# Optimization experiments

Hardware: AMD Instinct MI355X
Metric: run time of the kernel (lower is better)

The kernel has to match this reference:

```python
import jax, jax.numpy as jnp
import numpy as np

H, C, G, DIM = 8, 16, 32, 3
G3 = G ** 3
EPS = 1e-5
# corner offsets of the trilinear cell: [8, 3]
_OFFS = jnp.array([[i, j, k] for i in (0, 1) for j in (0, 1) for k in (0, 1)], dtype=jnp.int32)


def _bn(x, gamma, beta, mean, var):
    # eval-mode BatchNorm1d: x [B, Ch, N], params [Ch]
    inv = jax.lax.rsqrt(var + EPS)
    return (x - mean[:, None]) * (inv * gamma)[:, None] + beta[:, None]


def _lattice_coords(lattice):
    # lattice: [B, H, 3, N] in (-1, 1) -> flat indices [B,H,8,N], trilinear weights [B,H,8,N]
    pos = (lattice + 1.0) * (0.5 * (G - 1))
    base = jnp.clip(jnp.floor(pos), 0.0, G - 2)
    frac = pos - base                                   # [B,H,3,N]
    base = base.astype(jnp.int32)
    corner = base[:, :, None, :, :] + _OFFS[None, None, :, :, None]   # [B,H,8,3,N]
    flat_idx = (corner[:, :, :, 0] * G + corner[:, :, :, 1]) * G + corner[:, :, :, 2]
    w = jnp.where(_OFFS[None, None, :, :, None] == 1,
                  frac[:, :, None, :, :], 1.0 - frac[:, :, None, :, :])  # [B,H,8,3,N]
    weights = jnp.prod(w, axis=3)                       # [B,H,8,N]
    return flat_idx, weights


def _splat(values, flat_idx, weights):
    # values [B,H,C,N] -> lattice [B,H,C,G3] via weighted scatter-add over 8 corners
    N = values.shape[-1]
    def one(v, idx, w):  # v [C,N], idx/w [8,N]
        contrib = (v[:, None, :] * w[None, :, :]).reshape(C, 8 * N)
        return jnp.zeros((C, G3), v.dtype).at[:, idx.reshape(-1)].add(contrib)
    return jax.vmap(jax.vmap(one))(values, flat_idx, weights)


def _slice(grid, flat_idx, weights):
    # grid [B,H,C,G3] -> per-point features [B,H,C,N] via weighted gather over 8 corners
    N = flat_idx.shape[-1]
    def one(g, idx, w):
        gathered = g[:, idx.reshape(-1)].reshape(C, 8, N)
        return jnp.sum(gathered * w[None, :, :], axis=1)
    return jax.vmap(jax.vmap(one))(grid, flat_idx, weights)


def setup_inputs() -> dict:
    key = jax.random.key(0)
    ks = jax.random.split(key, 20)
    B, D, N = 4, 64, 16384
    inp = {
        "x": jax.random.normal(ks[0], (B, D, N), jnp.float32),
        "orig_points": jax.random.normal(ks[1], (B, 3, N), jnp.float32),
        "w_kv": jax.random.normal(ks[2], (H * (C + 3), D), jnp.float32) * 0.1,
        "kbn_gamma": jax.random.normal(ks[3], (H * 3,), jnp.float32) * 0.1,
        "kbn_beta": jax.random.normal(ks[4], (H * 3,), jnp.float32) * 0.1,
        "kbn_mean": jax.random.normal(ks[5], (H * 3,), jnp.float32) * 0.1,
        "kbn_var": jax.random.uniform(ks[6], (H * 3,), jnp.float32, 0.5, 1.5),
        "vbn_gamma": jax.random.normal(ks[7], (H * C,), jnp.float32),
        "vbn_beta": jax.random.normal(ks[8], (H * C,), jnp.float32) * 0.1,
        "vbn_mean": jax.random.normal(ks[9], (H * C,), jnp.float32) * 0.1,
        "vbn_var": jax.random.uniform(ks[10], (H * C,), jnp.float32, 0.5, 1.5),
        "Wt": jnp.eye(3, dtype=jnp.float32)[None] + jax.random.normal(ks[11], (H, 3, 3), jnp.float32) * 0.05,
        "bt": jax.random.normal(ks[12], (H, 3), jnp.float32) * 0.1,
        "conv_w": jax.random.normal(ks[13], (H * C, C, 3, 3, 3), jnp.float32) * 0.05,
        "conv_b": jax.random.normal(ks[14], (H * C,), jnp.float32) * 0.05,
        "abn_gamma": jax.random.normal(ks[15], (H * C,), jnp.float32),
        "abn_beta": jax.random.normal(ks[16], (H * C,), jnp.float32) * 0.1,
        "abn_mean": jax.random.normal(ks[17], (H * C,), jnp.float32) * 0.1,
        "abn_var": jax.random.uniform(ks[18], (H * C,), jnp.float32, 0.5, 1.5),
    }
    return inp


def reference(x, orig_points, w_kv, kbn_gamma, kbn_beta, kbn_mean, kbn_var,
              vbn_gamma, vbn_beta, vbn_mean, vbn_var, Wt, bt, conv_w, conv_b,
              abn_gamma, abn_beta, abn_mean, abn_var):
    B, D, N = x.shape
    kv = jnp.einsum('od,bdn->bon', w_kv, x)                       # [B, H*(C+3), N]
    keys_off = _bn(kv[:, :H * 3], kbn_gamma, kbn_beta, kbn_mean, kbn_var)
    values = _bn(kv[:, H * 3:], vbn_gamma, vbn_beta, vbn_mean, vbn_var)
    keys_off = keys_off.reshape(B, H, 3, N)
    pts = orig_points[:, None, :, :] + keys_off                   # [B,H,3,N]
    tkeys = jnp.einsum('hij,bhjn->bhin', Wt, pts) + bt[None, :, :, None]
    lattice = jnp.tanh(tkeys)                                     # [B,H,3,N]
    flat_idx, weights = _lattice_coords(lattice)
    vals = values.reshape(B, H, C, N)
    grid = _splat(vals, flat_idx, weights).reshape(B, H * C, G, G, G)
    conv = jax.lax.conv_general_dilated(
        grid, conv_w, (1, 1, 1), 'SAME',
        dimension_numbers=('NCDHW', 'OIDHW', 'NCDHW'),
        feature_group_count=H) + conv_b[None, :, None, None, None]
    sliced = _slice(conv.reshape(B, H, C, G3), flat_idx, weights)  # [B,H,C,N]
    out = _bn(sliced.reshape(B, H * C, N), abn_gamma, abn_beta, abn_mean, abn_var)
    return jax.nn.relu(out)
```

## Files before the change

### kernel.cpp

```cpp
#include <hip/hip_runtime.h>
#include <hip/hip_bf16.h>

#define NB  4
#define NH  8
#define NC  16
#define ND  64
#define NN  16384
#define NG  32
#define NG3 32768
#define NKV 152
#define KEPS 1e-5f
#define TN  256

typedef __attribute__((ext_vector_type(8))) short bf16x8;
typedef __attribute__((ext_vector_type(4))) float f32x4;

__device__ __forceinline__ unsigned pack_bf2(float lo, float hi) {
    __hip_bfloat16 a = __float2bfloat16(lo);
    __hip_bfloat16 b = __float2bfloat16(hi);
    return (unsigned)(*(unsigned short*)&a) | ((unsigned)(*(unsigned short*)&b) << 16);
}
__device__ __forceinline__ float bf_lo(unsigned u) { return __uint_as_float(u << 16); }
__device__ __forceinline__ float bf_hi(unsigned u) { return __uint_as_float(u & 0xffff0000u); }

__global__ __launch_bounds__(256)
void k_zero(uint4* __restrict__ p)
{
    p[(long)blockIdx.x * 256 + threadIdx.x] = make_uint4(0, 0, 0, 0);
}

__global__ __launch_bounds__(256)
void k_front4(const float* __restrict__ x,
              const float* __restrict__ orig,
              const float* __restrict__ wkv,
              const float* __restrict__ kg, const float* __restrict__ kb,
              const float* __restrict__ km, const float* __restrict__ kvv,
              const float* __restrict__ vg, const float* __restrict__ vb,
              const float* __restrict__ vm, const float* __restrict__ vv,
              const float* __restrict__ Wt,
              const float* __restrict__ bt,
              unsigned short* __restrict__ valb,
              float4* __restrict__ pre,
              int* __restrict__ hist)
{
    __shared__ unsigned short xb[TN * 72];
    __shared__ float wk[6 * ND];
    __shared__ float ksc[6], ksh[6], vsc[32], vsh[32], wts[18], bts[6];
    const int tid = threadIdx.x;
    const int hg   = blockIdx.x & 3;
    const int tile = (blockIdx.x >> 2) & 63;
    const int b    = blockIdx.x >> 8;
    const int n0 = tile * TN;
    const int n  = n0 + tid;

    for (int i = tid; i < 6 * ND; i += 256) wk[i] = wkv[hg * 384 + i];
    if (tid < 6) {
        int ch = hg * 6 + tid;
        float s = rsqrtf(kvv[ch] + KEPS) * kg[ch];
        ksc[tid] = s;
        ksh[tid] = kb[ch] - km[ch] * s;
    }
    if (tid < 32) {
        int ch = hg * 32 + tid;
        float s = rsqrtf(vv[ch] + KEPS) * vg[ch];
        vsc[tid] = s;
        vsh[tid] = vb[ch] - vm[ch] * s;
    }
    if (tid < 18) wts[tid] = Wt[hg * 18 + tid];
    if (tid < 6)  bts[tid] = bt[hg * 6 + tid];

    float xr[ND];
    #pragma unroll
    for (int d = 0; d < ND; ++d)
        xr[d] = x[((long)b * ND + d) * NN + n];
    #pragma unroll
    for (int j = 0; j < 8; ++j) {
        uint4 q;
        q.x = pack_bf2(xr[8*j+0], xr[8*j+1]);
        q.y = pack_bf2(xr[8*j+2], xr[8*j+3]);
        q.z = pack_bf2(xr[8*j+4], xr[8*j+5]);
        q.w = pack_bf2(xr[8*j+6], xr[8*j+7]);
        *(uint4*)(xb + tid * 72 + j * 8) = q;
    }
    __syncthreads();

    float ko[6];
    #pragma unroll 1
    for (int o = 0; o < 6; o += 3) {
        float s0 = 0.f, s1 = 0.f, s2 = 0.f;
        #pragma unroll
        for (int dq = 0; dq < 16; ++dq) {
            const float4 w0 = *(const float4*)&wk[(o + 0) * ND + dq * 4];
            const float4 w1 = *(const float4*)&wk[(o + 1) * ND + dq * 4];
            const float4 w2 = *(const float4*)&wk[(o + 2) * ND + dq * 4];
            float a0 = xr[4*dq], a1 = xr[4*dq+1], a2 = xr[4*dq+2], a3 = xr[4*dq+3];
            s0 = fmaf(w0.x, a0, fmaf(w0.y, a1, fmaf(w0.z, a2, fmaf(w0.w, a3, s0))));
            s1 = fmaf(w1.x, a0, fmaf(w1.y, a1, fmaf(w1.z, a2, fmaf(w1.w, a3, s1))));
            s2 = fmaf(w2.x, a0, fmaf(w2.y, a1, fmaf(w2.z, a2, fmaf(w2.w, a3, s2))));
        }
        ko[o + 0] = fmaf(s0, ksc[o + 0], ksh[o + 0]);
        ko[o + 1] = fmaf(s1, ksc[o + 1], ksh[o + 1]);
        ko[o + 2] = fmaf(s2, ksc[o + 2], ksh[o + 2]);
    }

    {
        const int lane = tid & 63;
        const int wv = tid >> 6;
        const int l15 = lane & 15, l4 = lane >> 4;
        const int hl = wv & 1;
        const int h = hg * 2 + hl;
        const int ocg = h * 16 + l15;
        const int nbr = (wv >> 1) * 8;
        const float bsc = vsc[hl * 16 + l15];
        const float bsh = vsh[hl * 16 + l15];

        bf16x8 bfr[2];
        #pragma unroll
        for (int ks = 0; ks < 2; ++ks) {
            const float* wp = wkv + (24 + ocg) * ND + ks * 32 + l4 * 8;
            float4 a = *(const float4*)wp;
            float4 c = *(const float4*)(wp + 4);
            uint4 q;
            q.x = pack_bf2(a.x, a.y); q.y = pack_bf2(a.z, a.w);
            q.z = pack_bf2(c.x, c.y); q.w = pack_bf2(c.z, c.w);
            bfr[ks] = *(bf16x8*)&q;
        }

        #pragma unroll 1
        for (int nbi = 0; nbi < 8; ++nbi) {
            int nb = nbr + nbi;
            bf16x8 a0 = *(const bf16x8*)(xb + (nb * 16 + l15) * 72 + l4 * 8);
            bf16x8 a1 = *(const bf16x8*)(xb + (nb * 16 + l15) * 72 + 32 + l4 * 8);
            f32x4 acc = (f32x4){0.f, 0.f, 0.f, 0.f};
            acc = __builtin_amdgcn_mfma_f32_16x16x32_bf16(a0, bfr[0], acc, 0, 0, 0);
            acc = __builtin_amdgcn_mfma_f32_16x16x32_bf16(a1, bfr[1], acc, 0, 0, 0);
            unsigned short* vp = valb + (((long)(b * NH + h) * NN + n0 + nb * 16 + l4 * 4) * NC) + l15;
            #pragma unroll
            for (int r = 0; r < 4; ++r) {
                __hip_bfloat16 hb = __float2bfloat16(fmaf(acc[r], bsc, bsh));
                vp[r * NC] = *(unsigned short*)&hb;
            }
        }
    }

    const float o0 = orig[((long)b * 3 + 0) * NN + n];
    const float o1 = orig[((long)b * 3 + 1) * NN + n];
    const float o2 = orig[((long)b * 3 + 2) * NN + n];

    #pragma unroll 1
    for (int lh = 0; lh < 2; ++lh) {
        float p0 = o0 + ko[lh * 3 + 0];
        float p1 = o1 + ko[lh * 3 + 1];
        float p2 = o2 + ko[lh * 3 + 2];
        float t0 = fmaf(wts[lh * 9 + 0], p0, fmaf(wts[lh * 9 + 1], p1, fmaf(wts[lh * 9 + 2], p2, bts[lh * 3 + 0])));
        float t1 = fmaf(wts[lh * 9 + 3], p0, fmaf(wts[lh * 9 + 4], p1, fmaf(wts[lh * 9 + 5], p2, bts[lh * 3 + 1])));
        float t2 = fmaf(wts[lh * 9 + 6], p0, fmaf(wts[lh * 9 + 7], p1, fmaf(wts[lh * 9 + 8], p2, bts[lh * 3 + 2])));
        float l0 = tanhf(t0), l1 = tanhf(t1), l2 = tanhf(t2);
        float pos0 = (l0 + 1.f) * 15.5f;
        float pos1 = (l1 + 1.f) * 15.5f;
        float pos2 = (l2 + 1.f) * 15.5f;
        float b0 = fminf(fmaxf(floorf(pos0), 0.f), 30.f);
        float b1 = fminf(fmaxf(floorf(pos1), 0.f), 30.f);
        float b2 = fminf(fmaxf(floorf(pos2), 0.f), 30.f);
        int ix = (int)b0, iy = (int)b1, iz = (int)b2;
        float fx = pos0 - b0, fy = pos1 - b1, fz = pos2 - b2;
        int ibase = (ix * NG + iy) * NG + iz;
        float4 pr;
        pr.x = __int_as_float(ibase);
        pr.y = fx; pr.z = fy; pr.w = fz;
        int bh = b * NH + hg * 2 + lh;
        pre[(long)bh * NN + n] = pr;
        atomicAdd(&hist[bh * NG3 + ibase], 1);
    }
}

__global__ __launch_bounds__(1024)
void k_scan_cells(const int* __restrict__ hist, int* __restrict__ offs,
                  int* __restrict__ offs_live)
{
    __shared__ int tsum[1024];
    const int bh = blockIdx.x, tid = threadIdx.x;
    const int* hb = hist + (long)bh * NG3;

    int s = 0;
    #pragma unroll 4
    for (int j = 0; j < 32; ++j) s += hb[tid * 32 + j];
    tsum[tid] = s;
    __syncthreads();
    for (int d = 1; d < 1024; d <<= 1) {
        int t = (tid >= d) ? tsum[tid - d] : 0;
        __syncthreads();
        tsum[tid] += t;
        __syncthreads();
    }
    int run = bh * NN + tsum[tid] - s;
    int* ob = offs + (long)bh * NG3;
    int* lb = offs_live + (long)bh * NG3;
    #pragma unroll 4
    for (int j = 0; j < 32; ++j) {
        int c = tid * 32 + j;
        ob[c] = run;
        lb[c] = run;
        run += hb[c];
    }
}

__global__ __launch_bounds__(256)
void k_scatter2(const float4* __restrict__ pre, const unsigned short* __restrict__ valb,
                int* __restrict__ offs_live, uint4* __restrict__ rec)
{
    const int bh   = 8 * ((blockIdx.x >> 3) & 3) + (blockIdx.x & 7);
    const int tile = blockIdx.x >> 5;
    long t = (long)bh * NN + tile * 256 + threadIdx.x;
    float4 r = pre[t];
    int ibase = __float_as_int(r.x);
    int slot = atomicAdd(&offs_live[(long)bh * NG3 + ibase], 1);
    const uint4* vp = (const uint4*)(valb + t * NC);
    uint4 v0 = vp[0], v1 = vp[1];
    uint4* out = rec + (long)slot * 3;
    out[0] = make_uint4(__float_as_uint(r.y), __float_as_uint(r.z), __float_as_uint(r.w), 0u);
    out[1] = v0;
    out[2] = v1;
}

__global__ __launch_bounds__(1024)
void k_splat6(const uint4* __restrict__ rec, const int* __restrict__ hist,
              const int* __restrict__ offs, unsigned short* __restrict__ gridb)
{
    __shared__ uint4 sr[1024 * 3];
    const int tid = threadIdx.x;
    const int bh = blockIdx.x & 31;
    const int rx = blockIdx.x >> 5;
    const int y = tid >> 5, z = tid & 31;
    const int zlo = (z > 0) ? z - 1 : 0;

    const int* hb = hist + (long)bh * NG3;
    const int* ob = offs + (long)bh * NG3;

    float acc[16];
    #pragma unroll
    for (int c = 0; c < 16; ++c) acc[c] = 0.f;

    #pragma unroll
    for (int dx = 0; dx < 2; ++dx) {
        int cx = rx - dx;
        if (cx < 0) continue;
        int st[2], sp[2], en[2];
        #pragma unroll
        for (int dy = 0; dy < 2; ++dy) {
            int cy = y - dy;
            bool valid = cy >= 0;
            int base = (cx << 10) | (cy << 5);
            int c1 = base | zlo;
            int c2 = base | z;
            st[dy] = valid ? ob[c1] : 0;
            sp[dy] = valid ? ob[c2] : 0;
            en[dy] = valid ? sp[dy] + hb[c2] : 0;
        }
        int pc0 = cx << 10;
        int ps = ob[pc0];
        int pe = ob[pc0 + 1023] + hb[pc0 + 1023];
        for (int cs = ps; cs < pe; cs += 1024) {
            int ce = min(cs + 1024, pe);
            __syncthreads();
            if (tid < ce - cs) {
                const uint4* R = rec + (long)(cs + tid) * 3;
                sr[tid * 3 + 0] = R[0];
                sr[tid * 3 + 1] = R[1];
                sr[tid * 3 + 2] = R[2];
            }
            __syncthreads();
            #pragma unroll
            for (int dy = 0; dy < 2; ++dy) {
                int ls = max(st[dy], cs);
                int le = min(en[dy], ce);
                int split = sp[dy];
                for (int r = ls; r < le; ++r) {
                    int k = (r - cs) * 3;
                    uint4 q0 = sr[k], q1 = sr[k + 1], q2 = sr[k + 2];
                    float fx = __uint_as_float(q0.x);
                    float fy = __uint_as_float(q0.y);
                    float fz = __uint_as_float(q0.z);
                    float wx = dx ? fx : 1.f - fx;
                    float wy = dy ? fy : 1.f - fy;
                    float wz = (r < split) ? fz : 1.f - fz;
                    float w = wx * wy * wz;
                    acc[0]  = fmaf(w, bf_lo(q1.x), acc[0]);
                    acc[1]  = fmaf(w, bf_hi(q1.x), acc[1]);
                    acc[2]  = fmaf(w, bf_lo(q1.y), acc[2]);
                    acc[3]  = fmaf(w, bf_hi(q1.y), acc[3]);
                    acc[4]  = fmaf(w, bf_lo(q1.z), acc[4]);
                    acc[5]  = fmaf(w, bf_hi(q1.z), acc[5]);
                    acc[6]  = fmaf(w, bf_lo(q1.w), acc[6]);
                    acc[7]  = fmaf(w, bf_hi(q1.w), acc[7]);
                    acc[8]  = fmaf(w, bf_lo(q2.x), acc[8]);
                    acc[9]  = fmaf(w, bf_hi(q2.x), acc[9]);
                    acc[10] = fmaf(w, bf_lo(q2.y), acc[10]);
                    acc[11] = fmaf(w, bf_hi(q2.y), acc[11]);
                    acc[12] = fmaf(w, bf_lo(q2.z), acc[12]);
                    acc[13] = fmaf(w, bf_hi(q2.z), acc[13]);
                    acc[14] = fmaf(w, bf_lo(q2.w), acc[14]);
                    acc[15] = fmaf(w, bf_hi(q2.w), acc[15]);
                }
            }
        }
    }

    uint4 q0, q1;
    q0.x = pack_bf2(acc[0],  acc[1]);  q0.y = pack_bf2(acc[2],  acc[3]);
    q0.z = pack_bf2(acc[4],  acc[5]);  q0.w = pack_bf2(acc[6],  acc[7]);
    q1.x = pack_bf2(acc[8],  acc[9]);  q1.y = pack_bf2(acc[10], acc[11]);
    q1.z = pack_bf2(acc[12], acc[13]); q1.w = pack_bf2(acc[14], acc[15]);
    uint4* gb = (uint4*)(gridb + ((long)bh * NG3 + (rx << 10) + tid) * NC);
    gb[0] = q0;
    gb[1] = q1;
}

__global__ __launch_bounds__(256)
void k_wprep(const float* __restrict__ cw, unsigned short* __restrict__ wpre)
{
    const int h = blockIdx.x;
    for (int e = threadIdx.x; e < 7168; e += 256) {
        int icl = e & 7, oc = (e >> 3) & 15, ihl = (e >> 7) & 1, tap = e >> 8;
        int ic = ihl * 8 + icl;
        float wv = (tap < 27) ? cw[(h * 16 + oc) * 432 + ic * 27 + tap] : 0.f;
        __hip_bfloat16 hbw = __float2bfloat16(wv);
        wpre[h * 7168 + e] = *(unsigned short*)&hbw;
    }
}

__global__ __launch_bounds__(512)
void k_conv5(const unsigned short* __restrict__ gridb,
             const unsigned short* __restrict__ wpre,
             const float* __restrict__ cb,
             unsigned short* __restrict__ convo)
{
    __shared__ unsigned short sg[2 * 6 * 10 * 34 * 8];
    __shared__ unsigned short sw[28 * 2 * 16 * 8];
    const int tid = threadIdx.x;
    const int bid = blockIdx.x;
    const int yt = bid & 3, xt = (bid >> 2) & 7, bh = bid >> 5;
    const int h = bh & 7;
    const int x0 = xt * 4, y0 = yt * 8;

    {
        const uint4* wsrc = (const uint4*)(wpre + (long)h * 7168);
        uint4* wdst = (uint4*)sw;
        for (int e = tid; e < 896; e += 512) wdst[e] = wsrc[e];
    }
    const unsigned short* gb = gridb + (long)bh * NG3 * 16;
    for (int e = tid; e < 2 * 6 * 10 * 34; e += 512) {
        int ihl = e & 1, c = e >> 1;
        int zz = c % 34, yu = c / 34;
        int yy = yu % 10, xx = yu / 10;
        int gx = x0 + xx - 1, gy = y0 + yy - 1, gz = zz - 1;
        uint4 v = make_uint4(0, 0, 0, 0);
        if ((unsigned)gx < NG && (unsigned)gy < NG && (unsigned)gz < NG)
            v = *(const uint4*)(gb + (((gx * NG + gy) * NG + gz) * 16 + ihl * 8));
        *(uint4*)(sg + ((((ihl * 6 + xx) * 10 + yy) * 34) + zz) * 8) = v;
    }
    __syncthreads();

    const int lane = tid & 63;
    const int w  = tid >> 6;
    const int wv = w & 3;
    const int zh = w >> 2;
    const int m  = lane & 15;
    const int l4 = lane >> 4;
    const int ihl = l4 & 1;
    const int tp = l4 >> 1;

    const int aLaneByte = ((((ihl * 6 + wv) * 10) * 34) + zh * 16 + m) * 16;
    const int bLaneByte = l4 * 256 + m * 16;
    const char* sgb = (const char*)sg;
    const char* swb = (const char*)sw;

    f32x4 acc[8];
    #pragma unroll
    for (int j = 0; j < 8; ++j) acc[j] = (f32x4){0.f, 0.f, 0.f, 0.f};

    #pragma unroll
    for (int p = 0; p < 14; ++p) {
        const int t0 = 2 * p, t1 = 2 * p + 1;
        const int ta0 = (t0 > 26) ? 26 : t0, ta1 = (t1 > 26) ? 26 : t1;
        const int off0 = ((ta0 / 9) * 340 + ((ta0 % 9) / 3) * 34 + (ta0 % 3)) * 16;
        const int off1 = ((ta1 / 9) * 340 + ((ta1 % 9) / 3) * 34 + (ta1 % 3)) * 16;
        const int aoff = aLaneByte + (tp ? off1 : off0);
        bf16x8 bfr = *(const bf16x8*)(swb + p * 1024 + bLaneByte);
        #pragma unroll
        for (int j = 0; j < 8; ++j) {
            bf16x8 afr = *(const bf16x8*)(sgb + aoff + j * 544);
            acc[j] = __builtin_amdgcn_mfma_f32_16x16x32_bf16(afr, bfr, acc[j], 0, 0, 0);
        }
    }

    const float bias = cb[h * 16 + m];
    unsigned short* cvb = convo + (long)bh * NG3 * NC;
    const int gx = x0 + wv;
    const int z0 = zh * 16;
    #pragma unroll
    for (int j = 0; j < 8; ++j) {
        int gy = y0 + j;
        long cellbase = (long)(gx * NG + gy) * NG + z0 + l4 * 4;
        #pragma unroll
        for (int r = 0; r < 4; ++r) {
            __hip_bfloat16 hb = __float2bfloat16(acc[j][r] + bias);
            cvb[(cellbase + r) * NC + m] = *(unsigned short*)&hb;
        }
    }
}

__global__ __launch_bounds__(256)
void k_slice(const unsigned short* __restrict__ convo, const float4* __restrict__ pre,
             const float* __restrict__ ag, const float* __restrict__ ab,
             const float* __restrict__ am, const float* __restrict__ av,
             float* __restrict__ out)
{
    __shared__ float asc[128], ash[128];
    const int tid = threadIdx.x;
    if (tid < 128) {
        float s = rsqrtf(av[tid] + KEPS) * ag[tid];
        asc[tid] = s;
        ash[tid] = ab[tid] - am[tid] * s;
    }
    __syncthreads();

    const int bh   = 8 * ((blockIdx.x >> 3) & 3) + (blockIdx.x & 7);
    const int tile = blockIdx.x >> 5;
    const int n = tile * 256 + tid;
    long t = (long)bh * NN + n;
    int b = bh >> 3, h = bh & 7;
    const unsigned short* g = convo + (long)bh * NG3 * NC;

    float4 r = pre[t];
    int ibase = __float_as_int(r.x);
    float fx = r.y, fy = r.z, fz = r.w;
    float gx = 1.f - fx, gy = 1.f - fy, gz = 1.f - fz;
    const float ws8[8] = {gx*gy*gz, gx*gy*fz, gx*fy*gz, gx*fy*fz,
                          fx*gy*gz, fx*gy*fz, fx*fy*gz, fx*fy*fz};
    const int offs8[8] = {0, 1, NG, NG + 1, NG*NG, NG*NG + 1, NG*NG + NG, NG*NG + NG + 1};

    float acc[NC];
    #pragma unroll
    for (int c = 0; c < NC; ++c) acc[c] = 0.f;
    #pragma unroll
    for (int ci = 0; ci < 8; ++ci) {
        float w = ws8[ci];
        const uint4* gc = (const uint4*)(g + (long)(ibase + offs8[ci]) * NC);
        uint4 u0 = gc[0], u1 = gc[1];
        acc[0]  = fmaf(w, bf_lo(u0.x), acc[0]);
        acc[1]  = fmaf(w, bf_hi(u0.x), acc[1]);
        acc[2]  = fmaf(w, bf_lo(u0.y), acc[2]);
        acc[3]  = fmaf(w, bf_hi(u0.y), acc[3]);
        acc[4]  = fmaf(w, bf_lo(u0.z), acc[4]);
        acc[5]  = fmaf(w, bf_hi(u0.z), acc[5]);
        acc[6]  = fmaf(w, bf_lo(u0.w), acc[6]);
        acc[7]  = fmaf(w, bf_hi(u0.w), acc[7]);
        acc[8]  = fmaf(w, bf_lo(u1.x), acc[8]);
        acc[9]  = fmaf(w, bf_hi(u1.x), acc[9]);
        acc[10] = fmaf(w, bf_lo(u1.y), acc[10]);
        acc[11] = fmaf(w, bf_hi(u1.y), acc[11]);
        acc[12] = fmaf(w, bf_lo(u1.z), acc[12]);
        acc[13] = fmaf(w, bf_hi(u1.z), acc[13]);
        acc[14] = fmaf(w, bf_lo(u1.w), acc[14]);
        acc[15] = fmaf(w, bf_hi(u1.w), acc[15]);
    }
    float* ob = out + ((long)b * 128 + h * 16) * NN + n;
    #pragma unroll
    for (int c = 0; c < NC; ++c) {
        float rr = fmaf(acc[c], asc[h * 16 + c], ash[h * 16 + c]);
        ob[(long)c * NN] = fmaxf(rr, 0.f);
    }
}

extern "C" void kernel_launch(void* const* d_in, const int* in_sizes, int n_in,
                              void* d_out, int out_size, void* d_ws, size_t ws_size,
                              hipStream_t stream)
{
    (void)in_sizes; (void)n_in; (void)out_size; (void)ws_size;
    const float* x    = (const float*)d_in[0];
    const float* orig = (const float*)d_in[1];
    const float* wkv  = (const float*)d_in[2];
    const float* kg   = (const float*)d_in[3];
    const float* kb   = (const float*)d_in[4];
    const float* km   = (const float*)d_in[5];
    const float* kvv  = (const float*)d_in[6];
    const float* vg   = (const float*)d_in[7];
    const float* vb   = (const float*)d_in[8];
    const float* vm   = (const float*)d_in[9];
    const float* vv   = (const float*)d_in[10];
    const float* Wt   = (const float*)d_in[11];
    const float* bt   = (const float*)d_in[12];
    const float* cw   = (const float*)d_in[13];
    const float* cb   = (const float*)d_in[14];
    const float* ag   = (const float*)d_in[15];
    const float* ab   = (const float*)d_in[16];
    const float* am   = (const float*)d_in[17];
    const float* av   = (const float*)d_in[18];

    char* ws = (char*)d_ws;
    float4*         pre       = (float4*)        (ws);
    int*            hist      = (int*)           (ws + 8388608);
    int*            offs      = (int*)           (ws + 12582912);
    int*            offs_live = (int*)           (ws + 16777216);
    unsigned short* valb      = (unsigned short*)(ws + 20971520);
    uint4*          rec       = (uint4*)         (ws + 37748736);
    unsigned short* gridb     = (unsigned short*)(ws + 62914560);
    unsigned short* wpre      = (unsigned short*)(ws + 96468992);
    unsigned short* convo     = (unsigned short*)(ws + 20971520);

    k_zero<<<dim3(1024), dim3(256), 0, stream>>>((uint4*)hist);

    k_wprep<<<dim3(NH), dim3(256), 0, stream>>>(cw, wpre);

    k_front4<<<dim3(NB * 256), dim3(256), 0, stream>>>(
        x, orig, wkv, kg, kb, km, kvv, vg, vb, vm, vv, Wt, bt, valb, pre, hist);

    k_scan_cells<<<dim3(NB * NH), dim3(1024), 0, stream>>>(hist, offs, offs_live);

    k_scatter2<<<dim3((NB * NH * NN) / 256), dim3(256), 0, stream>>>(
        pre, valb, offs_live, rec);

    k_splat6<<<dim3(NB * NH * NG), dim3(1024), 0, stream>>>(rec, hist, offs, gridb);

    k_conv5<<<dim3(NB * NH * 32), dim3(512), 0, stream>>>(gridb, wpre, cb, convo);

    k_slice<<<dim3((NB * NH * NN) / 256), dim3(256), 0, stream>>>(
        convo, pre, ag, ab, am, av, (float*)d_out);
}
```

Measured before the change: 195.6 us.

## Splat two x-planes per block to reuse loaded cell records

```diff
diff --git a/kernel.cpp b/kernel.cpp
--- a/kernel.cpp
+++ b/kernel.cpp
@@ -224,40 +224,42 @@
 }
 
 __global__ __launch_bounds__(1024)
-void k_splat6(const uint4* __restrict__ rec, const int* __restrict__ hist,
+void k_splat7(const uint4* __restrict__ rec, const int* __restrict__ hist,
               const int* __restrict__ offs, unsigned short* __restrict__ gridb)
 {
     __shared__ uint4 sr[1024 * 3];
     const int tid = threadIdx.x;
     const int bh = blockIdx.x & 31;
-    const int rx = blockIdx.x >> 5;
+    const int kp = blockIdx.x >> 5;
     const int y = tid >> 5, z = tid & 31;
     const int zlo = (z > 0) ? z - 1 : 0;
 
     const int* hb = hist + (long)bh * NG3;
     const int* ob = offs + (long)bh * NG3;
 
-    float acc[16];
-    #pragma unroll
-    for (int c = 0; c < 16; ++c) acc[c] = 0.f;
-
-    #pragma unroll
-    for (int dx = 0; dx < 2; ++dx) {
-        int cx = rx - dx;
-        if (cx < 0) continue;
+    float acc0[16], acc1[16];
+    #pragma unroll
+    for (int c = 0; c < 16; ++c) { acc0[c] = 0.f; acc1[c] = 0.f; }
+
+    #pragma unroll 1
+    for (int pi = 0; pi < 3; ++pi) {
+        int p = 2 * kp - 1 + pi;
+        if (p < 0) continue;
+        const bool u0 = (pi <= 1);
+        const bool u1 = (pi >= 1);
         int st[2], sp[2], en[2];
         #pragma unroll
         for (int dy = 0; dy < 2; ++dy) {
             int cy = y - dy;
             bool valid = cy >= 0;
-            int base = (cx << 10) | (cy << 5);
+            int base = (p << 10) | (cy << 5);
             int c1 = base | zlo;
             int c2 = base | z;
             st[dy] = valid ? ob[c1] : 0;
             sp[dy] = valid ? ob[c2] : 0;
             en[dy] = valid ? sp[dy] + hb[c2] : 0;
         }
-        int pc0 = cx << 10;
+        int pc0 = p << 10;
         int ps = ob[pc0];
         int pe = ob[pc0 + 1023] + hb[pc0 + 1023];
         for (int cs = ps; cs < pe; cs += 1024) {
@@ -281,39 +283,57 @@
                     float fx = __uint_as_float(q0.x);
                     float fy = __uint_as_float(q0.y);
                     float fz = __uint_as_float(q0.z);
-                    float wx = dx ? fx : 1.f - fx;
                     float wy = dy ? fy : 1.f - fy;
                     float wz = (r < split) ? fz : 1.f - fz;
-                    float w = wx * wy * wz;
-                    acc[0]  = fmaf(w, bf_lo(q1.x), acc[0]);
-                    acc[1]  = fmaf(w, bf_hi(q1.x), acc[1]);
-                    acc[2]  = fmaf(w, bf_lo(q1.y), acc[2]);
-                    acc[3]  = fmaf(w, bf_hi(q1.y), acc[3]);
-                    acc[4]  = fmaf(w, bf_lo(q1.z), acc[4]);
-                    acc[5]  = fmaf(w, bf_hi(q1.z), acc[5]);
-                    acc[6]  = fmaf(w, bf_lo(q1.w), acc[6]);
-                    acc[7]  = fmaf(w, bf_hi(q1.w), acc[7]);
-                    acc[8]  = fmaf(w, bf_lo(q2.x), acc[8]);
-                    acc[9]  = fmaf(w, bf_hi(q2.x), acc[9]);
-                    acc[10] = fmaf(w, bf_lo(q2.y), acc[10]);
-                    acc[11] = fmaf(w, bf_hi(q2.y), acc[11]);
-                    acc[12] = fmaf(w, bf_lo(q2.z), acc[12]);
-                    acc[13] = fmaf(w, bf_hi(q2.z), acc[13]);
-                    acc[14] = fmaf(w, bf_lo(q2.w), acc[14]);
-                    acc[15] = fmaf(w, bf_hi(q2.w), acc[15]);
+                    float wyz = wy * wz;
+                    float v[16];
+                    v[0]  = bf_lo(q1.x); v[1]  = bf_hi(q1.x);
+                    v[2]  = bf_lo(q1.y); v[3]  = bf_hi(q1.y);
+                    v[4]  = bf_lo(q1.z); v[5]  = bf_hi(q1.z);
+                    v[6]  = bf_lo(q1.w); v[7]  = bf_hi(q1.w);
+                    v[8]  = bf_lo(q2.x); v[9]  = bf_hi(q2.x);
+                    v[10] = bf_lo(q2.y); v[11] = bf_hi(q2.y);
+                    v[12] = bf_lo(q2.z); v[13] = bf_hi(q2.z);
+                    v[14] = bf_lo(q2.w); v[15] = bf_hi(q2.w);
+                    if (u0) {
+                        float wx0 = (pi == 0) ? fx : 1.f - fx;
+                        float w0 = wx0 * wyz;
+                        #pragma unroll
+                        for (int c = 0; c < 16; ++c)
+                            acc0[c] = fmaf(w0, v[c], acc0[c]);
+                    }
+                    if (u1) {
+                        float wx1 = (pi == 1) ? fx : 1.f - fx;
+                        float w1 = wx1 * wyz;
+                        #pragma unroll
+                        for (int c = 0; c < 16; ++c)
+                            acc1[c] = fmaf(w1, v[c], acc1[c]);
+                    }
                 }
             }
         }
     }
 
-    uint4 q0, q1;
-    q0.x = pack_bf2(acc[0],  acc[1]);  q0.y = pack_bf2(acc[2],  acc[3]);
-    q0.z = pack_bf2(acc[4],  acc[5]);  q0.w = pack_bf2(acc[6],  acc[7]);
-    q1.x = pack_bf2(acc[8],  acc[9]);  q1.y = pack_bf2(acc[10], acc[11]);
-    q1.z = pack_bf2(acc[12], acc[13]); q1.w = pack_bf2(acc[14], acc[15]);
-    uint4* gb = (uint4*)(gridb + ((long)bh * NG3 + (rx << 10) + tid) * NC);
-    gb[0] = q0;
-    gb[1] = q1;
+    {
+        uint4 q0, q1;
+        q0.x = pack_bf2(acc0[0],  acc0[1]);  q0.y = pack_bf2(acc0[2],  acc0[3]);
+        q0.z = pack_bf2(acc0[4],  acc0[5]);  q0.w = pack_bf2(acc0[6],  acc0[7]);
+        q1.x = pack_bf2(acc0[8],  acc0[9]);  q1.y = pack_bf2(acc0[10], acc0[11]);
+        q1.z = pack_bf2(acc0[12], acc0[13]); q1.w = pack_bf2(acc0[14], acc0[15]);
+        uint4* gb = (uint4*)(gridb + ((long)bh * NG3 + ((2 * kp) << 10) + tid) * NC);
+        gb[0] = q0;
+        gb[1] = q1;
+    }
+    {
+        uint4 q0, q1;
+        q0.x = pack_bf2(acc1[0],  acc1[1]);  q0.y = pack_bf2(acc1[2],  acc1[3]);
+        q0.z = pack_bf2(acc1[4],  acc1[5]);  q0.w = pack_bf2(acc1[6],  acc1[7]);
+        q1.x = pack_bf2(acc1[8],  acc1[9]);  q1.y = pack_bf2(acc1[10], acc1[11]);
+        q1.z = pack_bf2(acc1[12], acc1[13]); q1.w = pack_bf2(acc1[14], acc1[15]);
+        uint4* gb = (uint4*)(gridb + ((long)bh * NG3 + ((2 * kp + 1) << 10) + tid) * NC);
+        gb[0] = q0;
+        gb[1] = q1;
+    }
 }
 
 __global__ __launch_bounds__(256)
@@ -521,7 +541,7 @@
     k_scatter2<<<dim3((NB * NH * NN) / 256), dim3(256), 0, stream>>>(
         pre, valb, offs_live, rec);
 
-    k_splat6<<<dim3(NB * NH * NG), dim3(1024), 0, stream>>>(rec, hist, offs, gridb);
+    k_splat7<<<dim3(NB * NH * (NG / 2)), dim3(1024), 0, stream>>>(rec, hist, offs, gridb);
 
     k_conv5<<<dim3(NB * NH * 32), dim3(512), 0, stream>>>(gridb, wpre, cb, convo);
 
```

Result: no change. 197.2 us (+0.8%).
